# Optimization experiments

Hardware: AMD Instinct MI355X
Metric: run time of the kernel (lower is better)

Reference implementation:

```python
import jax, jax.numpy as jnp
import numpy as np

ROPE_BASE = 100.0  # croco/dust3r RoPE2D default freq


def _rope1d(tok, pos1d, base=ROPE_BASE):
    # tok: [B,H,N,D], pos1d: [B,N] int
    D = tok.shape[-1]
    half = D // 2
    inv_freq = 1.0 / (base ** (jnp.arange(0, D, 2, dtype=jnp.float32) / D))  # [D/2]
    ang = pos1d[..., None].astype(jnp.float32) * inv_freq                    # [B,N,D/2]
    ang = jnp.concatenate([ang, ang], axis=-1)                               # [B,N,D]
    cos = jnp.cos(ang)[:, None, :, :].astype(tok.dtype)  # [B,1,N,D]
    sin = jnp.sin(ang)[:, None, :, :].astype(tok.dtype)
    t1, t2 = tok[..., :half], tok[..., half:]
    rot = jnp.concatenate([-t2, t1], axis=-1)  # rotate_half
    return tok * cos + rot * sin


def rope2d(tok, pos, base=ROPE_BASE):
    # tok: [B,H,N,C], pos: [B,N,2] (y,x) integer coords
    D = tok.shape[-1] // 2
    y = _rope1d(tok[..., :D], pos[..., 0], base)
    x = _rope1d(tok[..., D:], pos[..., 1], base)
    return jnp.concatenate([y, x], axis=-1)


def setup_inputs() -> dict:
    key = jax.random.key(0)
    k1, k2, k3, k4, k5 = jax.random.split(key, 5)
    B, H, N, C = 2, 12, 2049, 64
    q = jax.random.normal(k1, (B, H, N, C), dtype=jnp.float32)
    k = jax.random.normal(k2, (B, H, N, C), dtype=jnp.float32)
    v = jax.random.normal(k3, (B, H, N, C), dtype=jnp.float32)
    qpos = jax.random.randint(k4, (B, N, 2), 0, 64, dtype=jnp.int32)
    kpos = jax.random.randint(k5, (B, N, 2), 0, 64, dtype=jnp.int32)
    mask_for_attention = jnp.ones((B, N, N), dtype=bool)
    return {"q": q, "k": k, "v": v, "qpos": qpos, "kpos": kpos,
            "mask_for_attention": mask_for_attention, "num_cls": 1}


def reference(q, k, v, qpos, kpos, mask_for_attention, num_cls):
    B, H, Nq, C = q.shape
    scale = C ** -0.5
    # split off cls tokens, apply RoPE only to positional tokens
    q_nc = rope2d(q[:, :, num_cls:], qpos[:, num_cls:])
    k_nc = rope2d(k[:, :, num_cls:], kpos[:, num_cls:])
    # block similarity matrix:
    #            | K_cls |   K_pos    |
    #   | Q_cls |        sim_qcls_k   |
    #   |       | sim_q |-------------|
    #   | Q_pos |        |  sim_rope  |
    sim_rope = jnp.einsum('bhqc,bhkc->bhqk', q_nc, k_nc)                      # [B,H,Nq-cls,Nk-cls]
    sim_qcls_k = jnp.einsum('bhqc,bhkc->bhqk', q[:, :, :num_cls], k[:, :, num_cls:])
    sim_q = jnp.einsum('bhqc,bhkc->bhqk', q, k[:, :, :num_cls])               # [B,H,Nq,cls]
    sim = jnp.concatenate([sim_qcls_k, sim_rope], axis=-2)
    sim = jnp.concatenate([sim_q, sim], axis=-1)                              # [B,H,Nq,Nk]
    sim = sim * scale
    sim = jnp.where(mask_for_attention[:, None], sim, -jnp.inf)
    attn = jax.nn.softmax(sim, axis=-1)
    x = jnp.einsum('bhqk,bhkc->bhqc', attn, v)
    return x.transpose(0, 2, 1, 3).reshape(B, Nq, C * H)
```

## Files before the change

### kernel.cpp

```cpp
#include <hip/hip_runtime.h>
#include <hip/hip_bf16.h>

typedef __attribute__((ext_vector_type(8))) short bf16x8;
typedef __attribute__((ext_vector_type(16))) float f32x16;
typedef __attribute__((ext_vector_type(4))) float f32x4;
typedef __attribute__((ext_vector_type(2))) float f32x2;
typedef unsigned short u16;

#define BN 2
#define HN 12
#define NN 2049
#define CN 64
#define NT 2048
#define BH 24
#define QSCL 0.1803368801111204f

__device__ __forceinline__ u16 f2bf(float x) {
  unsigned u = __builtin_bit_cast(unsigned, x);
  unsigned r = (u + 0x7fffu + ((u >> 16) & 1u)) >> 16;
  return (u16)r;
}

__device__ __forceinline__ unsigned cvt_pk(float lo, float hi) {
  unsigned r;
  asm("v_cvt_pk_bf16_f32 %0, %1, %2" : "=v"(r) : "v"(lo), "v"(hi));
  return r;
}

union PU {
  unsigned u[4];
  bf16x8 v;
};
union B8 {
  f32x2 h[2];
  bf16x8 v;
};

__global__ __launch_bounds__(256) void rope_pack(
    const float* __restrict__ q, const float* __restrict__ k, const float* __restrict__ v,
    const int* __restrict__ qpos, const int* __restrict__ kpos,
    u16* __restrict__ Qr, u16* __restrict__ Kr, u16* __restrict__ Vt,
    float* __restrict__ S0, float* __restrict__ Pl, float* __restrict__ Po) {
  const int bh = blockIdx.x;
  const int t = blockIdx.y;
  const int b = bh / HN;
  const int tid = threadIdx.x;
  const int wv = tid >> 6, l = tid & 63;

  __shared__ float lutc[1024], luts[1024];
  __shared__ u16 ldsV[64][36];
  __shared__ float q0s[64], k0s[64];
  __shared__ float osum[4][64];
  __shared__ float psum[4];

  const int n0 = 1 + t * 32;
  const size_t base0 = (size_t)bh * NN * CN;

  const float LF = 6.6438561897747253f / 16.0f;
  for (int i = tid; i < 1024; i += 256) {
    const int pos = i >> 4, f = i & 15;
    const float inv = exp2f(-(float)f * LF);
    float sv, cv;
    sincosf((float)pos * inv, &sv, &cv);
    lutc[i] = cv;
    luts[i] = sv;
  }
  if (tid < 64) {
    q0s[tid] = q[base0 + tid];
    k0s[tid] = k[base0 + tid];
  }
  __syncthreads();

  float oacc = 0.f, pacc = 0.f;
#pragma unroll 2
  for (int i = 0; i < 8; ++i) {
    const int tok = i * 4 + wv;
    const int c = l;
    const int n = n0 + tok;
    const size_t base = base0 + (size_t)n * CN;
    const int cp = c & 31, f = cp & 15, axis = c >> 5;
    const int qp_ = qpos[((size_t)b * NN + n) * 2 + axis];
    const int kp_ = kpos[((size_t)b * NN + n) * 2 + axis];
    const float qa = q[base + c];
    const float ka = k[base + c];
    const float qrot = (cp < 16) ? -q[base + c + 16] : q[base + c - 16];
    const float krot = (cp < 16) ? -k[base + c + 16] : k[base + c - 16];
    Qr[((size_t)bh * NT + (n - 1)) * CN + c] =
        f2bf((qa * lutc[qp_ * 16 + f] + qrot * luts[qp_ * 16 + f]) * QSCL);
    const int rsw = ((n - 1) & 15) << 2;
    Kr[((size_t)bh * NT + (n - 1)) * CN + (c ^ rsw)] =
        f2bf(ka * lutc[kp_ * 16 + f] + krot * luts[kp_ * 16 + f]);
    const float vv = v[base + c];
    ldsV[c][tok] = f2bf(vv);

    float pk = ka * q0s[c];
    float pq = qa * k0s[c];
    pk += __shfl_xor(pk, 1, 64);  pq += __shfl_xor(pq, 1, 64);
    pk += __shfl_xor(pk, 2, 64);  pq += __shfl_xor(pq, 2, 64);
    pk += __shfl_xor(pk, 4, 64);  pq += __shfl_xor(pq, 4, 64);
    pk += __shfl_xor(pk, 8, 64);  pq += __shfl_xor(pq, 8, 64);
    pk += __shfl_xor(pk, 16, 64); pq += __shfl_xor(pq, 16, 64);
    pk += __shfl_xor(pk, 32, 64); pq += __shfl_xor(pq, 32, 64);
    const float p = __builtin_amdgcn_exp2f(pk * QSCL);
    pacc += p;
    oacc += p * vv;
    if (l == 0) S0[(size_t)bh * NT + (n - 1)] = pq * QSCL;
  }
  osum[wv][l] = oacc;
  if (l == 0) psum[wv] = pacc;
  __syncthreads();

  for (int e = tid; e < 2048; e += 256) {
    const int c = e >> 5, tok = e & 31;
    const int T = t * 32 + tok;
    const int t6 = T & 63, ch = t6 >> 3, j = t6 & 7;
    const int pos = 16 * (ch >> 1) + 4 * (ch & 1) + 8 * (j >> 2) + (j & 3);
    Vt[((size_t)bh * CN + c) * NT + (T >> 6) * 64 + (pos ^ ((c & 15) << 2))] = ldsV[c][tok];
  }
  if (tid < 64)
    Po[(size_t)(bh * 64 + t) * 64 + tid] =
        osum[0][tid] + osum[1][tid] + osum[2][tid] + osum[3][tid];
  if (tid == 0) Pl[bh * 64 + t] = psum[0] + psum[1] + psum[2] + psum[3];
}

__global__ __launch_bounds__(64) void row0_reduce(
    const float* __restrict__ q, const float* __restrict__ k, const float* __restrict__ v,
    const float* __restrict__ Pl, const float* __restrict__ Po, float* __restrict__ out) {
  const int bh = blockIdx.x;
  const int b = bh / HN, h = bh % HN;
  const int c = threadIdx.x;
  const size_t base0 = (size_t)bh * NN * CN;
  float pr = q[base0 + c] * k[base0 + c];
  pr += __shfl_xor(pr, 1, 64);
  pr += __shfl_xor(pr, 2, 64);
  pr += __shfl_xor(pr, 4, 64);
  pr += __shfl_xor(pr, 8, 64);
  pr += __shfl_xor(pr, 16, 64);
  pr += __shfl_xor(pr, 32, 64);
  const float p00 = __builtin_amdgcn_exp2f(pr * QSCL);
  float L = p00;
  float acc = p00 * v[base0 + c];
#pragma unroll
  for (int i = 0; i < 64; ++i) {
    L += Pl[bh * 64 + i];
    acc += Po[(size_t)(bh * 64 + i) * 64 + c];
  }
  out[(size_t)b * NN * (HN * CN) + h * CN + c] = acc / L;
}

__global__ __launch_bounds__(256, 3) void attn_main(
    const float* __restrict__ v,
    const u16* __restrict__ Qr, const u16* __restrict__ Kr, const u16* __restrict__ Vt,
    const float* __restrict__ S0, float* __restrict__ out) {
  const int wg = blockIdx.x;
  const int bh = 3 * (wg & 7) + ((wg >> 3) >> 5);
  const int qt = (wg >> 3) & 31;
  const int b = bh / HN, h = bh % HN;
  const int tid = threadIdx.x;
  const int wv = tid >> 6, l = tid & 63;
  const int l31 = l & 31, lh = l >> 5;
  const int qh = wv & 1, kh = wv >> 1;

  __shared__ u16 ldsK[2][4096];
  __shared__ u16 ldsV[2][4096];
  __shared__ float v0f[64];
  __shared__ float Lbuf[64];
  float* Obuf = reinterpret_cast<float*>(&ldsK[0][0]);

  if (tid < 64) v0f[tid] = v[(size_t)bh * NN * CN + tid];
  __syncthreads();

  const int qrow = qt * 64 + qh * 32 + l31;
  const u16* qp = Qr + ((size_t)bh * NT + qrow) * CN + lh * 8;
  bf16x8 qf[4];
#pragma unroll
  for (int s = 0; s < 4; ++s) qf[s] = *reinterpret_cast<const bf16x8*>(qp + s * 16);

  const float s0l2 = S0[(size_t)bh * NT + qrow];
  const float p0 = __builtin_amdgcn_exp2f(s0l2);
  float lsum = (kh == 0 && lh == 0) ? p0 : 0.f;

  f32x16 o[2];
#pragma unroll
  for (int half = 0; half < 2; ++half)
#pragma unroll
    for (int reg = 0; reg < 16; ++reg)
      o[half][reg] =
          (kh == 0) ? p0 * v0f[(reg & 3) + 8 * (reg >> 2) + 4 * lh + 32 * half] : 0.f;

  const u16* Kbh = Kr + (size_t)bh * NT * CN;
  const u16* Vbh = Vt + (size_t)bh * CN * NT;
  char* ldsKc = reinterpret_cast<char*>(&ldsK[0][0]);
  char* ldsVc = reinterpret_cast<char*>(&ldsV[0][0]);

  const int s16 = tid & 7, srowA = tid >> 3, srowB = (tid >> 3) + 32;

#define DMA_TILE(nx, bofs)                                                                   \
  do {                                                                                       \
    __builtin_amdgcn_global_load_lds(                                                        \
        (const __attribute__((address_space(1))) unsigned int*)(Kbh +                        \
            (size_t)((nx) + srowA) * CN + s16 * 8),                                          \
        (__attribute__((address_space(3))) unsigned int*)(ldsKc + (bofs) + wv * 1024),       \
        16, 0, 0);                                                                           \
    __builtin_amdgcn_global_load_lds(                                                        \
        (const __attribute__((address_space(1))) unsigned int*)(Kbh +                        \
            (size_t)((nx) + srowB) * CN + s16 * 8),                                          \
        (__attribute__((address_space(3))) unsigned int*)(ldsKc + (bofs) + 4096 + wv * 1024),\
        16, 0, 0);                                                                           \
    __builtin_amdgcn_global_load_lds(                                                        \
        (const __attribute__((address_space(1))) unsigned int*)(Vbh +                        \
            (size_t)srowA * NT + (nx) + s16 * 8),                                            \
        (__attribute__((address_space(3))) unsigned int*)(ldsVc + (bofs) + wv * 1024),       \
        16, 0, 0);                                                                           \
    __builtin_amdgcn_global_load_lds(                                                        \
        (const __attribute__((address_space(1))) unsigned int*)(Vbh +                        \
            (size_t)srowB * NT + (nx) + s16 * 8),                                            \
        (__attribute__((address_space(3))) unsigned int*)(ldsVc + (bofs) + 4096 + wv * 1024),\
        16, 0, 0);                                                                           \
  } while (0)

  DMA_TILE(0, 0);

#pragma unroll 2
  for (int kt = 0; kt < 32; ++kt) {
    const int cur = (kt & 1) * 8192;
    const int nxt = ((kt + 1) & 1) * 8192;
    __syncthreads();
    if (kt < 31) DMA_TILE((kt + 1) * 64, nxt);

    const int trow = kh * 32 + l31;
    const int tsw = (trow & 15) << 3;
    f32x16 S;
#pragma unroll
    for (int reg = 0; reg < 16; ++reg) S[reg] = 0.f;
    __builtin_amdgcn_s_setprio(1);
#pragma unroll
    for (int st = 0; st < 4; ++st) {
      B8 kb;
      const int cb = st * 32 + lh * 16;
      kb.h[0] = *reinterpret_cast<const f32x2*>(ldsKc + cur + trow * 128 + (cb ^ tsw));
      kb.h[1] = *reinterpret_cast<const f32x2*>(ldsKc + cur + trow * 128 + ((cb + 8) ^ tsw));
      S = __builtin_amdgcn_mfma_f32_32x32x16_bf16(kb.v, qf[st], S, 0, 0, 0);
    }
    __builtin_amdgcn_s_setprio(0);

    PU pa[2];
    {
      float e[16];
#pragma unroll
      for (int reg = 0; reg < 16; ++reg) e[reg] = __builtin_amdgcn_exp2f(S[reg]);
#pragma unroll
      for (int reg = 0; reg < 16; reg += 4)
        lsum += (e[reg] + e[reg + 1]) + (e[reg + 2] + e[reg + 3]);
#pragma unroll
      for (int m = 0; m < 4; ++m) {
        pa[0].u[m] = cvt_pk(e[2 * m], e[2 * m + 1]);
        pa[1].u[m] = cvt_pk(e[8 + 2 * m], e[9 + 2 * m]);
      }
    }

    __builtin_amdgcn_s_setprio(1);
#pragma unroll
    for (int half = 0; half < 2; ++half) {
      const int crow = half * 32 + l31;
      const int csw = (crow & 15) << 3;
#pragma unroll
      for (int ks = 0; ks < 2; ++ks) {
        B8 vb;
        const int pb = (kh * 2 + ks) * 32 + lh * 16;
        vb.h[0] = *reinterpret_cast<const f32x2*>(ldsVc + cur + crow * 128 + (pb ^ csw));
        vb.h[1] = *reinterpret_cast<const f32x2*>(ldsVc + cur + crow * 128 + ((pb + 8) ^ csw));
        o[half] = __builtin_amdgcn_mfma_f32_32x32x16_bf16(vb.v, pa[ks].v, o[half], 0, 0, 0);
      }
    }
    __builtin_amdgcn_s_setprio(0);
  }

  const float wls = lsum + __shfl_xor(lsum, 32, 64);
  __syncthreads();
  if (kh == 1) {
#pragma unroll
    for (int half = 0; half < 2; ++half)
#pragma unroll
      for (int reg = 0; reg < 16; ++reg) {
        const int c = (reg & 3) + 8 * (reg >> 2) + 4 * lh + 32 * half;
        Obuf[qh * 2048 + c * 32 + l31] = o[half][reg];
      }
    if (lh == 0) Lbuf[qh * 32 + l31] = wls;
  }
  __syncthreads();
  if (kh == 0) {
    const float L = wls + Lbuf[qh * 32 + l31];
    const float invl = 1.0f / L;
    const int n = 1 + qrow;
    float* op = out + ((size_t)b * NN + n) * (HN * CN) + h * CN;
#pragma unroll
    for (int half = 0; half < 2; ++half) {
#pragma unroll
      for (int rg = 0; rg < 4; ++rg) {
        f32x4 val;
#pragma unroll
        for (int j = 0; j < 4; ++j) {
          const int reg = 4 * rg + j;
          const int c = (reg & 3) + 8 * (reg >> 2) + 4 * lh + 32 * half;
          val[j] = (o[half][reg] + Obuf[qh * 2048 + c * 32 + l31]) * invl;
        }
        *reinterpret_cast<f32x4*>(op + 8 * rg + 4 * lh + 32 * half) = val;
      }
    }
  }
#undef DMA_TILE
}

extern "C" void kernel_launch(void* const* d_in, const int* in_sizes, int n_in,
                              void* d_out, int out_size, void* d_ws, size_t ws_size,
                              hipStream_t stream) {
  const float* q = (const float*)d_in[0];
  const float* k = (const float*)d_in[1];
  const float* v = (const float*)d_in[2];
  const int* qpos = (const int*)d_in[3];
  const int* kpos = (const int*)d_in[4];
  float* out = (float*)d_out;

  u16* Qr = (u16*)d_ws;
  u16* Kr = Qr + (size_t)BH * NT * CN;
  u16* Vt = Kr + (size_t)BH * NT * CN;
  float* S0 = (float*)(Vt + (size_t)BH * NT * CN);
  float* Pl = S0 + (size_t)BH * NT;
  float* Po = Pl + BH * 64;

  rope_pack<<<dim3(BH, 64), 256, 0, stream>>>(q, k, v, qpos, kpos, Qr, Kr, Vt, S0, Pl, Po);
  attn_main<<<dim3(BH * 32), 256, 0, stream>>>(v, Qr, Kr, Vt, S0, out);
  row0_reduce<<<dim3(BH), 64, 0, stream>>>(q, k, v, Pl, Po, out);
}
```

Baseline: 61.09 us.

## Software-pipeline QK of next tile with PV of current tile using triple-buffered K

Restructures the attention main loop so the QK^T product and exp for tile kt+1 are computed in the same iteration as the PV product for tile kt. K gets a three-stage LDS ring buffer and is prefetched two tiles ahead, while V stays double-buffered one tile ahead. The aim is to let the exp/pack VALU work overlap with the MFMA work and to hide load latency better. In exchange, LDS use rises by 8 KB per block, which may cut occupancy under launch_bounds(256,3), and register pressure goes up because pa is carried across iterations.

```diff
diff --git a/kernel.cpp b/kernel.cpp
--- a/kernel.cpp
+++ b/kernel.cpp
@@ -161,7 +161,7 @@
   const int l31 = l & 31, lh = l >> 5;
   const int qh = wv & 1, kh = wv >> 1;
 
-  __shared__ u16 ldsK[2][4096];
+  __shared__ u16 ldsK[3][4096];
   __shared__ u16 ldsV[2][4096];
   __shared__ float v0f[64];
   __shared__ float Lbuf[64];
@@ -195,85 +195,117 @@
 
   const int s16 = tid & 7, srowA = tid >> 3, srowB = (tid >> 3) + 32;
 
-#define DMA_TILE(nx, bofs)                                                                   \
-  do {                                                                                       \
-    __builtin_amdgcn_global_load_lds(                                                        \
-        (const __attribute__((address_space(1))) unsigned int*)(Kbh +                        \
-            (size_t)((nx) + srowA) * CN + s16 * 8),                                          \
-        (__attribute__((address_space(3))) unsigned int*)(ldsKc + (bofs) + wv * 1024),       \
-        16, 0, 0);                                                                           \
-    __builtin_amdgcn_global_load_lds(                                                        \
-        (const __attribute__((address_space(1))) unsigned int*)(Kbh +                        \
-            (size_t)((nx) + srowB) * CN + s16 * 8),                                          \
-        (__attribute__((address_space(3))) unsigned int*)(ldsKc + (bofs) + 4096 + wv * 1024),\
-        16, 0, 0);                                                                           \
-    __builtin_amdgcn_global_load_lds(                                                        \
-        (const __attribute__((address_space(1))) unsigned int*)(Vbh +                        \
-            (size_t)srowA * NT + (nx) + s16 * 8),                                            \
-        (__attribute__((address_space(3))) unsigned int*)(ldsVc + (bofs) + wv * 1024),       \
-        16, 0, 0);                                                                           \
-    __builtin_amdgcn_global_load_lds(                                                        \
-        (const __attribute__((address_space(1))) unsigned int*)(Vbh +                        \
-            (size_t)srowB * NT + (nx) + s16 * 8),                                            \
-        (__attribute__((address_space(3))) unsigned int*)(ldsVc + (bofs) + 4096 + wv * 1024),\
-        16, 0, 0);                                                                           \
-  } while (0)
-
-  DMA_TILE(0, 0);
-
-#pragma unroll 2
-  for (int kt = 0; kt < 32; ++kt) {
-    const int cur = (kt & 1) * 8192;
-    const int nxt = ((kt + 1) & 1) * 8192;
-    __syncthreads();
-    if (kt < 31) DMA_TILE((kt + 1) * 64, nxt);
-
-    const int trow = kh * 32 + l31;
-    const int tsw = (trow & 15) << 3;
+#define DMA_K(nx, bofs)                                                                       \
+  do {                                                                                        \
+    __builtin_amdgcn_global_load_lds(                                                         \
+        (const __attribute__((address_space(1))) unsigned int*)(Kbh +                         \
+            (size_t)((nx) + srowA) * CN + s16 * 8),                                           \
+        (__attribute__((address_space(3))) unsigned int*)(ldsKc + (bofs) + wv * 1024),        \
+        16, 0, 0);                                                                            \
+    __builtin_amdgcn_global_load_lds(                                                         \
+        (const __attribute__((address_space(1))) unsigned int*)(Kbh +                         \
+            (size_t)((nx) + srowB) * CN + s16 * 8),                                           \
+        (__attribute__((address_space(3))) unsigned int*)(ldsKc + (bofs) + 4096 + wv * 1024), \
+        16, 0, 0);                                                                            \
+  } while (0)
+
+#define DMA_V(nx, bofs)                                                                       \
+  do {                                                                                        \
+    __builtin_amdgcn_global_load_lds(                                                         \
+        (const __attribute__((address_space(1))) unsigned int*)(Vbh +                         \
+            (size_t)srowA * NT + (nx) + s16 * 8),                                             \
+        (__attribute__((address_space(3))) unsigned int*)(ldsVc + (bofs) + wv * 1024),        \
+        16, 0, 0);                                                                            \
+    __builtin_amdgcn_global_load_lds(                                                         \
+        (const __attribute__((address_space(1))) unsigned int*)(Vbh +                         \
+            (size_t)srowB * NT + (nx) + s16 * 8),                                             \
+        (__attribute__((address_space(3))) unsigned int*)(ldsVc + (bofs) + 4096 + wv * 1024), \
+        16, 0, 0);                                                                            \
+  } while (0)
+
+  const int trow = kh * 32 + l31;
+  const int tsw = (trow & 15) << 3;
+
+#define QK_TILE(S, bofs)                                                                      \
+  do {                                                                                        \
+    _Pragma("unroll") for (int st = 0; st < 4; ++st) {                                        \
+      B8 kb;                                                                                  \
+      const int cb = st * 32 + lh * 16;                                                       \
+      kb.h[0] = *reinterpret_cast<const f32x2*>(ldsKc + (bofs) + trow * 128 + (cb ^ tsw));    \
+      kb.h[1] =                                                                               \
+          *reinterpret_cast<const f32x2*>(ldsKc + (bofs) + trow * 128 + ((cb + 8) ^ tsw));    \
+      S = __builtin_amdgcn_mfma_f32_32x32x16_bf16(kb.v, qf[st], S, 0, 0, 0);                  \
+    }                                                                                         \
+  } while (0)
+
+#define EXP_PACK(S, pa)                                                                       \
+  do {                                                                                        \
+    float e[16];                                                                              \
+    _Pragma("unroll") for (int r2 = 0; r2 < 16; ++r2)                                         \
+        e[r2] = __builtin_amdgcn_exp2f(S[r2]);                                                \
+    _Pragma("unroll") for (int r2 = 0; r2 < 16; r2 += 4)                                      \
+        lsum += (e[r2] + e[r2 + 1]) + (e[r2 + 2] + e[r2 + 3]);                                \
+    _Pragma("unroll") for (int m = 0; m < 4; ++m) {                                           \
+      pa[0].u[m] = cvt_pk(e[2 * m], e[2 * m + 1]);                                            \
+      pa[1].u[m] = cvt_pk(e[8 + 2 * m], e[9 + 2 * m]);                                        \
+    }                                                                                         \
+  } while (0)
+
+#define PV_TILE(pa, bofs)                                                                     \
+  do {                                                                                        \
+    _Pragma("unroll") for (int half = 0; half < 2; ++half) {                                  \
+      const int crow = half * 32 + l31;                                                       \
+      const int csw = (crow & 15) << 3;                                                       \
+      _Pragma("unroll") for (int ks = 0; ks < 2; ++ks) {                                      \
+        B8 vb;                                                                                \
+        const int pb = (kh * 2 + ks) * 32 + lh * 16;                                          \
+        vb.h[0] =                                                                             \
+            *reinterpret_cast<const f32x2*>(ldsVc + (bofs) + crow * 128 + (pb ^ csw));        \
+        vb.h[1] =                                                                             \
+            *reinterpret_cast<const f32x2*>(ldsVc + (bofs) + crow * 128 + ((pb + 8) ^ csw));  \
+        o[half] = __builtin_amdgcn_mfma_f32_32x32x16_bf16(vb.v, pa[ks].v, o[half], 0, 0, 0);  \
+      }                                                                                       \
+    }                                                                                         \
+  } while (0)
+
+  DMA_K(0, 0);
+  DMA_K(64, 8192);
+  DMA_V(0, 0);
+  __syncthreads();
+  PU pa[2];
+  {
     f32x16 S;
 #pragma unroll
     for (int reg = 0; reg < 16; ++reg) S[reg] = 0.f;
     __builtin_amdgcn_s_setprio(1);
-#pragma unroll
-    for (int st = 0; st < 4; ++st) {
-      B8 kb;
-      const int cb = st * 32 + lh * 16;
-      kb.h[0] = *reinterpret_cast<const f32x2*>(ldsKc + cur + trow * 128 + (cb ^ tsw));
-      kb.h[1] = *reinterpret_cast<const f32x2*>(ldsKc + cur + trow * 128 + ((cb + 8) ^ tsw));
-      S = __builtin_amdgcn_mfma_f32_32x32x16_bf16(kb.v, qf[st], S, 0, 0, 0);
+    QK_TILE(S, 0);
+    __builtin_amdgcn_s_setprio(0);
+    EXP_PACK(S, pa);
+  }
+
+  int kw = 16384;
+  int kr = 8192;
+  for (int kt = 0; kt < 32; ++kt) {
+    __syncthreads();
+    if (kt < 30) DMA_K((kt + 2) * 64, kw);
+    if (kt < 31) DMA_V((kt + 1) * 64, ((kt + 1) & 1) * 8192);
+
+    const int vcur = (kt & 1) * 8192;
+    __builtin_amdgcn_s_setprio(1);
+    PV_TILE(pa, vcur);
+    if (kt < 31) {
+      f32x16 S;
+#pragma unroll
+      for (int reg = 0; reg < 16; ++reg) S[reg] = 0.f;
+      QK_TILE(S, kr);
+      __builtin_amdgcn_s_setprio(0);
+      EXP_PACK(S, pa);
+    } else {
+      __builtin_amdgcn_s_setprio(0);
     }
-    __builtin_amdgcn_s_setprio(0);
-
-    PU pa[2];
-    {
-      float e[16];
-#pragma unroll
-      for (int reg = 0; reg < 16; ++reg) e[reg] = __builtin_amdgcn_exp2f(S[reg]);
-#pragma unroll
-      for (int reg = 0; reg < 16; reg += 4)
-        lsum += (e[reg] + e[reg + 1]) + (e[reg + 2] + e[reg + 3]);
-#pragma unroll
-      for (int m = 0; m < 4; ++m) {
-        pa[0].u[m] = cvt_pk(e[2 * m], e[2 * m + 1]);
-        pa[1].u[m] = cvt_pk(e[8 + 2 * m], e[9 + 2 * m]);
-      }
-    }
-
-    __builtin_amdgcn_s_setprio(1);
-#pragma unroll
-    for (int half = 0; half < 2; ++half) {
-      const int crow = half * 32 + l31;
-      const int csw = (crow & 15) << 3;
-#pragma unroll
-      for (int ks = 0; ks < 2; ++ks) {
-        B8 vb;
-        const int pb = (kh * 2 + ks) * 32 + lh * 16;
-        vb.h[0] = *reinterpret_cast<const f32x2*>(ldsVc + cur + crow * 128 + (pb ^ csw));
-        vb.h[1] = *reinterpret_cast<const f32x2*>(ldsVc + cur + crow * 128 + ((pb + 8) ^ csw));
-        o[half] = __builtin_amdgcn_mfma_f32_32x32x16_bf16(vb.v, pa[ks].v, o[half], 0, 0, 0);
-      }
-    }
-    __builtin_amdgcn_s_setprio(0);
+
+    kw = (kw == 16384) ? 0 : kw + 8192;
+    kr = (kr == 16384) ? 0 : kr + 8192;
   }
 
   const float wls = lsum + __shfl_xor(lsum, 32, 64);
@@ -309,7 +341,11 @@
       }
     }
   }
-#undef DMA_TILE
+#undef DMA_K
+#undef DMA_V
+#undef QK_TILE
+#undef EXP_PACK
+#undef PV_TILE
 }
 
 extern "C" void kernel_launch(void* const* d_in, const int* in_sizes, int n_in,
```

Measured after the change: 63.06 us. 1.03x slower.
